# Optimization experiments

Hardware: AMD Instinct MI355X
Metric: run time of the kernel (lower is better)

Reference implementation:

```python
import jax, jax.numpy as jnp
import numpy as np

LN_EPS = 1e-5
DELTA_FACTOR = 0.01
PATCH_KH, PATCH_KW = 4, 4
SIGMA = 2.0


def layernorm(x, g, b):
    m = jnp.mean(x, axis=-1, keepdims=True)
    v = jnp.var(x, axis=-1, keepdims=True)
    return (x - m) * jax.lax.rsqrt(v + LN_EPS) * g + b


def grid_sample(src, grid):
    # src [B,C,H,W], grid [B,Hg,Wg,2] in [-1,1]; bilinear, align_corners=False, zero padding
    B, C, H, W = src.shape
    Hg, Wg = grid.shape[1], grid.shape[2]
    gx = (grid[..., 0] + 1.0) * (W * 0.5) - 0.5
    gy = (grid[..., 1] + 1.0) * (H * 0.5) - 0.5
    x0 = jnp.floor(gx)
    y0 = jnp.floor(gy)
    wx = gx - x0
    wy = gy - y0
    x0i = x0.astype(jnp.int32)
    y0i = y0.astype(jnp.int32)
    flat = src.reshape(B, C, H * W)

    def tap(xi, yi, w):
        valid = (xi >= 0) & (xi < W) & (yi >= 0) & (yi < H)
        idx = (jnp.clip(yi, 0, H - 1) * W + jnp.clip(xi, 0, W - 1)).reshape(B, -1)
        vals = jax.vmap(lambda f, i: f[:, i])(flat, idx)  # [B,C,Hg*Wg]
        return vals * (w * valid).reshape(B, 1, -1)

    out = (tap(x0i, y0i, (1 - wx) * (1 - wy)) + tap(x0i + 1, y0i, wx * (1 - wy))
           + tap(x0i, y0i + 1, (1 - wx) * wy) + tap(x0i + 1, y0i + 1, wx * wy))
    return out.reshape(B, C, Hg, Wg)


def gaussian_filt(x, k, sigma):
    # depthwise Gaussian blur, NCHW
    C = x.shape[1]
    coords = jnp.arange(k, dtype=x.dtype) - (k - 1) / 2.0
    g2 = jnp.exp(-(coords[:, None] ** 2 + coords[None, :] ** 2) / (2.0 * sigma ** 2))
    g2 = g2 / g2.sum()
    kern = jnp.broadcast_to(g2, (C, 1, k, k))
    p = (k - 1) // 2
    return jax.lax.conv_general_dilated(x, kern, (1, 1), [(p, p), (p, p)],
                                        dimension_numbers=('NCHW', 'OIHW', 'NCHW'),
                                        feature_group_count=C)


def reconstruct_feature(feature, mask, k, sigma):
    if k <= 1:
        return feature
    feature = feature * mask
    out = gaussian_filt(jnp.concatenate([feature, mask], axis=1), k, sigma)
    f_i = out[:, :-1]
    m_i = out[:, -1:]
    f_i = f_i / (m_i + 1e-6)
    f_i = f_i * (m_i > 0)
    return feature + (1 - mask) * f_i


def token2map(x, loc, H, W, k, sigma):
    B, N, C = x.shape
    l = jnp.clip(loc, 0.0, 1.0) * jnp.array([W - 1, H - 1], dtype=loc.dtype)
    l = jnp.round(l).astype(jnp.int32)
    idx = l[..., 0] + l[..., 1] * W + (jnp.arange(B, dtype=jnp.int32) * (H * W))[:, None]
    vals = jnp.concatenate([x, jnp.ones((B, N, 1), x.dtype)], axis=-1).reshape(B * N, C + 1)
    out = jnp.zeros((B * H * W, C + 1), x.dtype).at[idx.reshape(-1)].add(vals)
    out = out.reshape(B, H, W, C + 1).transpose(0, 3, 1, 2)
    feat, mask = out[:, :-1], out[:, -1:]
    feat = feat / (mask + 1e-6)
    mask = (mask > 0).astype(x.dtype)
    feat = feat * mask
    return reconstruct_feature(feat, mask, k, sigma)


def forward(x, loc, src, H, W, kernel_size,
            w_delta, b_delta, norm1_g, norm1_b, conv_w, conv_b,
            norm2_g, norm2_b, fc1_w, fc1_b, fc2_w, fc2_b):
    B, N, _ = loc.shape
    Cs, Hs, Ws = src.shape[1], src.shape[2], src.shape[3]
    delta = (layernorm(x, norm1_g, norm1_b) @ w_delta + b_delta) * DELTA_FACTOR
    loc_extra = jnp.clip(loc + delta, 0.0, 1.0)
    # extract_local_feature: 4x4 sub-pixel patch around each extra location
    xo = (jnp.arange(PATCH_KW, dtype=loc.dtype) - (PATCH_KW - 1) / 2.0) / (Ws - 1)
    yo = (jnp.arange(PATCH_KH, dtype=loc.dtype) - (PATCH_KH - 1) / 2.0) / (Hs - 1)
    off = jnp.stack([jnp.broadcast_to(xo[None, :], (PATCH_KH, PATCH_KW)),
                     jnp.broadcast_to(yo[:, None], (PATCH_KH, PATCH_KW))], axis=-1)
    grid = (loc_extra[:, :, None, None, :] + off[None, None]) * 2.0 - 1.0  # [B,N,kh,kw,2]
    patches = grid_sample(src, grid.reshape(B, N, PATCH_KH * PATCH_KW, 2))  # [B,C,N,kh*kw]
    patches = patches.reshape(B, Cs, N, PATCH_KH, PATCH_KW)
    # local_conv: 4x4 conv stride 4 over a 4x4 patch == single dot product
    extra = jnp.einsum('bcnhw,ochw->bno', patches, conv_w) + conv_b
    extra = layernorm(extra, norm2_g, norm2_b)
    # token2map scatter + gaussian reconstruction, then gather back at loc_extra
    fmap = token2map(x, loc, H, W, kernel_size, SIGMA)
    extra_inter = grid_sample(fmap, (loc_extra * 2.0 - 1.0)[:, None, :, :])  # [B,C,1,N]
    extra_inter = extra_inter[:, :, 0].transpose(0, 2, 1)  # [B,N,C]
    extra = jnp.concatenate([extra_inter, extra], axis=-1)
    h = jax.nn.gelu(extra @ fc1_w + fc1_b, approximate=False)
    extra = h @ fc2_w + fc2_b
    return jnp.concatenate([x, extra], axis=1), jnp.concatenate([loc, loc_extra], axis=1)


def setup_inputs() -> dict:
    key = jax.random.key(0)
    ks = jax.random.split(key, 12)
    B, N, D = 4, 16384, 256
    LD, HID = 64, 4 * D
    inp = {
        'x': jax.random.normal(ks[0], (B, N, D), jnp.float32),
        'loc': jax.random.uniform(ks[1], (B, N, 2), jnp.float32),
        'src': jax.random.normal(ks[2], (B, 3, 512, 512), jnp.float32),
        'pos_embed': jnp.zeros((1,), jnp.float32),
        'H': 128, 'W': 128, 'kernel_size': 3,
        'w_delta': jax.random.normal(ks[3], (D, 2), jnp.float32) * 0.02,
        'b_delta': jnp.zeros((2,), jnp.float32),
        'norm1_g': jnp.ones((D,), jnp.float32),
        'norm1_b': jnp.zeros((D,), jnp.float32),
        'conv_w': jax.random.normal(ks[4], (LD, 3, 4, 4), jnp.float32) * 0.1,
        'conv_b': jnp.zeros((LD,), jnp.float32),
        'norm2_g': jnp.ones((LD,), jnp.float32),
        'norm2_b': jnp.zeros((LD,), jnp.float32),
        'fc1_w': jax.random.normal(ks[5], (D + LD, HID), jnp.float32) * 0.02,
        'fc1_b': jnp.zeros((HID,), jnp.float32),
        'fc2_w': jax.random.normal(ks[6], (HID, D), jnp.float32) * 0.02,
        'fc2_b': jnp.zeros((D,), jnp.float32),
    }
    return inp


def reference(x, loc, src, pos_embed, H, W, kernel_size,
              w_delta, b_delta, norm1_g, norm1_b, conv_w, conv_b,
              norm2_g, norm2_b, fc1_w, fc1_b, fc2_w, fc2_b):
    # pos_embed is accepted by the torch forward but never used
    return forward(x, loc, src, H, W, kernel_size,
                   w_delta, b_delta, norm1_g, norm1_b, conv_w, conv_b,
                   norm2_g, norm2_b, fc1_w, fc1_b, fc2_w, fc2_b)
```

## Files before the change

kernel.cpp:

```cpp
#include <hip/hip_runtime.h>
#include <hip/hip_bf16.h>

#define B_    4
#define N_    16384
#define D_    256
#define LD_   64
#define HID_  1024
#define HW_   128
#define HSRC_ 512
#define CS_   3
#define KIN_  320

typedef __attribute__((ext_vector_type(8))) short bf16x8;
typedef __attribute__((ext_vector_type(4))) float f32x4;

__device__ __forceinline__ float wsum(float v) {
#pragma unroll
  for (int off = 32; off; off >>= 1) v += __shfl_xor(v, off, 64);
  return v;
}

__device__ __forceinline__ unsigned short f2bf(float f) {
  unsigned int u = __float_as_uint(f);
  u = (u + 0x7fffu + ((u >> 16) & 1u)) >> 16;
  return (unsigned short)u;
}

__global__ __launch_bounds__(256) void k_wconv(const float* __restrict__ fc1w,
                                               const float* __restrict__ fc2w,
                                               unsigned short* __restrict__ bt1,
                                               unsigned short* __restrict__ bt2) {
  int i = blockIdx.x * 256 + threadIdx.x;
  if (i < KIN_ * HID_) {
    int n = i / KIN_, k = i % KIN_;
    bt1[i] = f2bf(fc1w[(size_t)k * HID_ + n]);
  } else {
    int j = i - KIN_ * HID_;
    if (j < D_ * HID_) {
      int n = j / HID_, k = j % HID_;
      bt2[j] = f2bf(fc2w[(size_t)k * D_ + n]);
    }
  }
}

__global__ __launch_bounds__(256) void k_copy_x(const float* __restrict__ x,
                                                float* __restrict__ out0) {
  size_t i = (size_t)blockIdx.x * 256 + threadIdx.x;
  size_t e = i * 4;
  size_t b = e / ((size_t)N_ * D_);
  size_t off = e - b * (size_t)N_ * D_;
  *(float4*)(out0 + b * (size_t)2 * N_ * D_ + off) = *(const float4*)(x + e);
}

__global__ __launch_bounds__(256) void k_delta(const float* __restrict__ x,
                                               const float* __restrict__ loc,
                                               const float* __restrict__ wd,
                                               const float* __restrict__ bd,
                                               const float* __restrict__ g1,
                                               const float* __restrict__ b1,
                                               float* __restrict__ locex,
                                               float* __restrict__ out1) {
  int wv = threadIdx.x >> 6, lane = threadIdx.x & 63;
  int t = blockIdx.x * 4 + wv;
  const float4 xv = *(const float4*)(x + (size_t)t * D_ + lane * 4);
  float m = wsum(xv.x + xv.y + xv.z + xv.w) * (1.0f / D_);
  float d0 = xv.x - m, d1 = xv.y - m, d2 = xv.z - m, d3 = xv.w - m;
  float v = wsum(d0 * d0 + d1 * d1 + d2 * d2 + d3 * d3) * (1.0f / D_);
  float r = rsqrtf(v + 1e-5f);
  const float4 gv = *(const float4*)(g1 + lane * 4);
  const float4 bv = *(const float4*)(b1 + lane * 4);
  float n0 = d0 * r * gv.x + bv.x;
  float n1 = d1 * r * gv.y + bv.y;
  float n2 = d2 * r * gv.z + bv.z;
  float n3 = d3 * r * gv.w + bv.w;
  int i2 = lane * 8;
  float p0 = n0 * wd[i2 + 0] + n1 * wd[i2 + 2] + n2 * wd[i2 + 4] + n3 * wd[i2 + 6];
  float p1 = n0 * wd[i2 + 1] + n1 * wd[i2 + 3] + n2 * wd[i2 + 5] + n3 * wd[i2 + 7];
  p0 = wsum(p0);
  p1 = wsum(p1);
  if (lane == 0) {
    float lx = loc[(size_t)t * 2], ly = loc[(size_t)t * 2 + 1];
    float ex = fminf(fmaxf(lx + (p0 + bd[0]) * 0.01f, 0.0f), 1.0f);
    float ey = fminf(fmaxf(ly + (p1 + bd[1]) * 0.01f, 0.0f), 1.0f);
    locex[(size_t)t * 2] = ex;
    locex[(size_t)t * 2 + 1] = ey;
    int b = t >> 14, n = t & (N_ - 1);
    size_t o1 = (size_t)b * 2 * N_;
    out1[(o1 + n) * 2 + 0] = lx;
    out1[(o1 + n) * 2 + 1] = ly;
    out1[(o1 + N_ + n) * 2 + 0] = ex;
    out1[(o1 + N_ + n) * 2 + 1] = ey;
  }
}

__global__ __launch_bounds__(256) void k_build(const float* __restrict__ loc,
                                               int* __restrict__ head,
                                               int* __restrict__ nxt) {
  int t = blockIdx.x * 256 + threadIdx.x;
  int b = t >> 14;
  float lx = fminf(fmaxf(loc[(size_t)t * 2], 0.0f), 1.0f) * 127.0f;
  float ly = fminf(fmaxf(loc[(size_t)t * 2 + 1], 0.0f), 1.0f) * 127.0f;
  int ix = (int)rintf(lx);
  int iy = (int)rintf(ly);
  int cell = (b << 14) + iy * HW_ + ix;
  nxt[t] = atomicExch(head + cell, t);
}

__global__ __launch_bounds__(256) void k_gather(const float* __restrict__ x,
                                                const int* __restrict__ head,
                                                const int* __restrict__ nxt,
                                                float* __restrict__ featn,
                                                float* __restrict__ cntf) {
  int cell = blockIdx.x;
  int tid = threadIdx.x;
  __shared__ int toks[16];
  __shared__ int scount, snext;
  float acc = 0.0f;
  int total = 0;
  int cur = head[cell];
  while (cur >= 0) {
    if (tid == 0) {
      int c = 0, p = cur;
      while (p >= 0 && c < 16) {
        toks[c++] = p;
        p = nxt[p];
      }
      scount = c;
      snext = p;
    }
    __syncthreads();
    int c = scount;
    for (int i = 0; i < c; ++i) acc += x[(size_t)toks[i] * D_ + tid];
    total += c;
    cur = snext;
    __syncthreads();
  }
  featn[(size_t)cell * D_ + tid] = (total > 0) ? acc / ((float)total + 1e-6f) : 0.0f;
  if (tid == 0) cntf[cell] = (float)total;
}

__global__ __launch_bounds__(256) void k_filter(const float* __restrict__ featn,
                                                const float* __restrict__ cntf,
                                                float* __restrict__ fmap) {
  int pix = blockIdx.x;
  int c = threadIdx.x;
  int b = pix >> 14;
  int p = pix & 16383;
  int y = p >> 7, xc = p & 127;
  float cc = cntf[pix];
  float outv;
  if (cc > 0.0f) {
    outv = featn[(size_t)pix * D_ + c];
  } else {
    float e1 = expf(-0.125f), e2 = expf(-0.25f);
    float sumw = 1.0f + 4.0f * e1 + 4.0f * e2;
    float gf = 0.0f, gm = 0.0f;
#pragma unroll
    for (int dy = -1; dy <= 1; ++dy)
#pragma unroll
      for (int dx = -1; dx <= 1; ++dx) {
        int ny = y + dy, nx = xc + dx;
        if (ny < 0 || ny >= HW_ || nx < 0 || nx >= HW_) continue;
        int q = (b << 14) + ny * HW_ + nx;
        if (cntf[q] > 0.0f) {
          int dd = dy * dy + dx * dx;
          float w = (dd == 0 ? 1.0f : (dd == 1 ? e1 : e2)) / sumw;
          gf += w * featn[(size_t)q * D_ + c];
          gm += w;
        }
      }
    outv = (gm > 0.0f) ? gf / (gm + 1e-6f) : 0.0f;
  }
  fmap[(size_t)pix * D_ + c] = outv;
}

__global__ __launch_bounds__(256) void k_patch(const float* __restrict__ src,
                                               const float* __restrict__ locex,
                                               const float* __restrict__ convw,
                                               const float* __restrict__ convb,
                                               const float* __restrict__ g2,
                                               const float* __restrict__ b2,
                                               unsigned short* __restrict__ ecat) {
  __shared__ float cw[LD_ * 49];
  __shared__ float patch[4][48];
  for (int i = threadIdx.x; i < LD_ * 48; i += 256)
    cw[(i / 48) * 49 + (i % 48)] = convw[i];
  int wv = threadIdx.x >> 6, lane = threadIdx.x & 63;
  int t = blockIdx.x * 4 + wv;
  int b = t >> 14;
  float ex = locex[(size_t)t * 2], ey = locex[(size_t)t * 2 + 1];
  __syncthreads();
  if (lane < 48) {
    int c = lane >> 4, p = lane & 15, py = p >> 2, px = p & 3;
    float u = ex + ((float)px - 1.5f) / 511.0f;
    float vv = ey + ((float)py - 1.5f) / 511.0f;
    float gx = u * 512.0f - 0.5f;
    float gy = vv * 512.0f - 0.5f;
    float fx = floorf(gx), fy = floorf(gy);
    float wx = gx - fx, wy = gy - fy;
    int x0 = (int)fx, y0 = (int)fy;
    const float* plane = src + (size_t)(b * CS_ + c) * (HSRC_ * HSRC_);
    float acc = 0.0f;
#pragma unroll
    for (int ty = 0; ty < 2; ++ty)
#pragma unroll
      for (int tx = 0; tx < 2; ++tx) {
        int xi = x0 + tx, yi = y0 + ty;
        float w = (tx ? wx : 1.0f - wx) * (ty ? wy : 1.0f - wy);
        if (xi >= 0 && xi < HSRC_ && yi >= 0 && yi < HSRC_)
          acc += w * plane[yi * HSRC_ + xi];
      }
    patch[wv][lane] = acc;
  }
  __syncthreads();
  float e = convb[lane];
#pragma unroll
  for (int i = 0; i < 48; ++i) e += patch[wv][i] * cw[lane * 49 + i];
  float m = wsum(e) * (1.0f / 64.0f);
  float d = e - m;
  float v = wsum(d * d) * (1.0f / 64.0f);
  float val = d * rsqrtf(v + 1e-5f) * g2[lane] + b2[lane];
  ecat[(size_t)t * KIN_ + D_ + lane] = f2bf(val);
}

__global__ __launch_bounds__(256) void k_sample(const float* __restrict__ fmap,
                                                const float* __restrict__ locex,
                                                unsigned short* __restrict__ ecat) {
  int wv = threadIdx.x >> 6, lane = threadIdx.x & 63;
  int t = blockIdx.x * 4 + wv;
  int b = t >> 14;
  float gx = locex[(size_t)t * 2] * 128.0f - 0.5f;
  float gy = locex[(size_t)t * 2 + 1] * 128.0f - 0.5f;
  float fx = floorf(gx), fy = floorf(gy);
  float wx = gx - fx, wy = gy - fy;
  int x0 = (int)fx, y0 = (int)fy;
  const float* base = fmap + ((size_t)b << 14) * D_;
  float4 acc = {0.0f, 0.0f, 0.0f, 0.0f};
#pragma unroll
  for (int ty = 0; ty < 2; ++ty)
#pragma unroll
    for (int tx = 0; tx < 2; ++tx) {
      int xi = x0 + tx, yi = y0 + ty;
      float w = (tx ? wx : 1.0f - wx) * (ty ? wy : 1.0f - wy);
      if (xi >= 0 && xi < HW_ && yi >= 0 && yi < HW_) {
        const float4 f = *(const float4*)(base + (size_t)(yi * HW_ + xi) * D_ + lane * 4);
        acc.x += w * f.x;
        acc.y += w * f.y;
        acc.z += w * f.z;
        acc.w += w * f.w;
      }
    }
  ushort4 o;
  o.x = f2bf(acc.x);
  o.y = f2bf(acc.y);
  o.z = f2bf(acc.z);
  o.w = f2bf(acc.w);
  *(ushort4*)(ecat + (size_t)t * KIN_ + lane * 4) = o;
}

template <int GELU>
__global__ __launch_bounds__(256) void k_gemm(const unsigned short* __restrict__ A,
                                              const unsigned short* __restrict__ Bt,
                                              const float* __restrict__ bias, int K,
                                              int Nn, unsigned short* __restrict__ hout,
                                              float* __restrict__ out0) {
  __shared__ __align__(16) unsigned short As[64 * 40];
  __shared__ __align__(16) unsigned short Bs[64 * 40];
  int tid = threadIdx.x, wv = tid >> 6, lane = tid & 63;
  int tile_m = blockIdx.x * 64, tile_n = blockIdx.y * 64;
  int lr = tid >> 2, lc = (tid & 3) * 8;
  f32x4 acc[4];
#pragma unroll
  for (int s = 0; s < 4; ++s) acc[s] = (f32x4){0.0f, 0.0f, 0.0f, 0.0f};
  int arow = wv * 16 + (lane & 15);
  int kk = (lane >> 4) * 8;
  for (int k0 = 0; k0 < K; k0 += 32) {
    *(uint4*)(&As[lr * 40 + lc]) = *(const uint4*)(A + (size_t)(tile_m + lr) * K + k0 + lc);
    *(uint4*)(&Bs[lr * 40 + lc]) = *(const uint4*)(Bt + (size_t)(tile_n + lr) * K + k0 + lc);
    __syncthreads();
    bf16x8 af = *(const bf16x8*)(&As[arow * 40 + kk]);
#pragma unroll
    for (int s = 0; s < 4; ++s) {
      bf16x8 bfv = *(const bf16x8*)(&Bs[(s * 16 + (lane & 15)) * 40 + kk]);
      acc[s] = __builtin_amdgcn_mfma_f32_16x16x32_bf16(af, bfv, acc[s], 0, 0, 0);
    }
    __syncthreads();
  }
  int mbase = tile_m + wv * 16 + (lane >> 4) * 4;
#pragma unroll
  for (int s = 0; s < 4; ++s) {
    int n = tile_n + s * 16 + (lane & 15);
    float bv = bias[n];
#pragma unroll
    for (int r = 0; r < 4; ++r) {
      int m = mbase + r;
      float v = acc[s][r] + bv;
      if (GELU) {
        v = 0.5f * v * (1.0f + erff(v * 0.70710678118654752f));
        hout[(size_t)m * Nn + n] = f2bf(v);
      } else {
        int bb = m >> 14, ntok = m & (N_ - 1);
        out0[((size_t)bb * 2 * N_ + N_ + ntok) * D_ + n] = v;
      }
    }
  }
}

extern "C" void kernel_launch(void* const* d_in, const int* in_sizes, int n_in,
                              void* d_out, int out_size, void* d_ws, size_t ws_size,
                              hipStream_t stream) {
  const float* x = (const float*)d_in[0];
  const float* loc = (const float*)d_in[1];
  const float* src = (const float*)d_in[2];
  const float* wd = (const float*)d_in[7];
  const float* bd = (const float*)d_in[8];
  const float* g1 = (const float*)d_in[9];
  const float* b1 = (const float*)d_in[10];
  const float* cw = (const float*)d_in[11];
  const float* cb = (const float*)d_in[12];
  const float* g2 = (const float*)d_in[13];
  const float* b2 = (const float*)d_in[14];
  const float* fc1w = (const float*)d_in[15];
  const float* fc1b = (const float*)d_in[16];
  const float* fc2w = (const float*)d_in[17];
  const float* fc2b = (const float*)d_in[18];

  float* out0 = (float*)d_out;
  float* out1 = out0 + (size_t)B_ * 2 * N_ * D_;

  char* ws = (char*)d_ws;
  float* featn = (float*)(ws + 0);
  float* fmap = (float*)(ws + 67108864);
  unsigned short* h = (unsigned short*)(ws + 0);
  float* cntf = (float*)(ws + 134217728);
  float* locex = (float*)(ws + 134479872);
  unsigned short* ecat = (unsigned short*)(ws + 135004160);
  unsigned short* bt1 = (unsigned short*)(ws + 176947200);
  unsigned short* bt2 = (unsigned short*)(ws + 177602560);
  int* head = (int*)(ws + 178126848);
  int* nxt = (int*)(ws + 178388992);

  hipMemsetAsync(head, 0xFF, (size_t)262144, stream);

  k_wconv<<<2304, 256, 0, stream>>>(fc1w, fc2w, bt1, bt2);
  k_copy_x<<<16384, 256, 0, stream>>>(x, out0);
  k_delta<<<16384, 256, 0, stream>>>(x, loc, wd, bd, g1, b1, locex, out1);
  k_build<<<256, 256, 0, stream>>>(loc, head, nxt);
  k_gather<<<65536, 256, 0, stream>>>(x, head, nxt, featn, cntf);
  k_filter<<<65536, 256, 0, stream>>>(featn, cntf, fmap);
  k_patch<<<16384, 256, 0, stream>>>(src, locex, cw, cb, g2, b2, ecat);
  k_sample<<<16384, 256, 0, stream>>>(fmap, locex, ecat);
  k_gemm<1><<<dim3(1024, 16), 256, 0, stream>>>(ecat, bt1, fc1b, KIN_, HID_, h, nullptr);
  k_gemm<0><<<dim3(1024, 4), 256, 0, stream>>>(h, bt2, fc2b, HID_, D_, nullptr, out0);
}
```

Before: 665.4 us.

## Use 128x128 MFMA GEMM tiles with direct global-to-LDS loads and XCD-aware tile mapping

Replaces the 64x64 GEMM tile, where each wave computes a 16x64 strip, with a 128x128 tile in which each wave computes a 64x64 sub-block of 4x4 MFMA fragments. This raises arithmetic intensity per LDS load. Global-to-shared copies now use the global_load_lds builtin to skip register staging, and block indices are remapped so that consecutive M tiles land on the same XCD for L2 reuse. The trade-offs are higher register pressure and an unpadded LDS layout that may cause bank conflicts.

Result: faster. 592.0 us (-11.0%).

```diff
diff --git a/kernel.cpp b/kernel.cpp
--- a/kernel.cpp
+++ b/kernel.cpp
@@ -24,6 +24,12 @@
   unsigned int u = __float_as_uint(f);
   u = (u + 0x7fffu + ((u >> 16) & 1u)) >> 16;
   return (unsigned short)u;
+}
+
+__device__ __forceinline__ void async16(unsigned short* lds, const unsigned short* g) {
+  __builtin_amdgcn_global_load_lds(
+      (const __attribute__((address_space(1))) unsigned int*)g,
+      (__attribute__((address_space(3))) unsigned int*)lds, 16, 0, 0);
 }
 
 __global__ __launch_bounds__(256) void k_wconv(const float* __restrict__ fc1w,
@@ -259,48 +265,83 @@
 }
 
 template <int GELU>
-__global__ __launch_bounds__(256) void k_gemm(const unsigned short* __restrict__ A,
-                                              const unsigned short* __restrict__ Bt,
-                                              const float* __restrict__ bias, int K,
-                                              int Nn, unsigned short* __restrict__ hout,
-                                              float* __restrict__ out0) {
-  __shared__ __align__(16) unsigned short As[64 * 40];
-  __shared__ __align__(16) unsigned short Bs[64 * 40];
+__global__ __launch_bounds__(256) void k_gemm128(const unsigned short* __restrict__ A,
+                                                 const unsigned short* __restrict__ Bt,
+                                                 const float* __restrict__ bias, int K,
+                                                 int Nn, unsigned short* __restrict__ hout,
+                                                 float* __restrict__ out0) {
+  __shared__ __align__(16) unsigned short As[128 * 32];
+  __shared__ __align__(16) unsigned short Bs[128 * 32];
   int tid = threadIdx.x, wv = tid >> 6, lane = tid & 63;
-  int tile_m = blockIdx.x * 64, tile_n = blockIdx.y * 64;
-  int lr = tid >> 2, lc = (tid & 3) * 8;
-  f32x4 acc[4];
-#pragma unroll
-  for (int s = 0; s < 4; ++s) acc[s] = (f32x4){0.0f, 0.0f, 0.0f, 0.0f};
-  int arow = wv * 16 + (lane & 15);
+  int wm = wv & 1, wn = wv >> 1;
+
+  int nt_cnt = gridDim.x;
+  int lin = blockIdx.y * nt_cnt + blockIdx.x;
+  int xcd = lin & 7;
+  int slot = lin >> 3;
+  int tile_n = (slot % nt_cnt) * 128;
+  int tile_m = ((slot / nt_cnt) * 8 + xcd) * 128;
+
+  f32x4 acc[4][4];
+#pragma unroll
+  for (int i = 0; i < 4; ++i)
+#pragma unroll
+    for (int j = 0; j < 4; ++j) acc[i][j] = (f32x4){0.0f, 0.0f, 0.0f, 0.0f};
+
+  int r0 = tid >> 2, c0 = (tid & 3) * 8;
+  const unsigned short* ga = A + (size_t)(tile_m + r0) * K + c0;
+  const unsigned short* gb = Bt + (size_t)(tile_n + r0) * K + c0;
+  size_t rowskip = (size_t)64 * K;
+  unsigned short* lA0 = As + tid * 8;
+  unsigned short* lA1 = As + 2048 + tid * 8;
+  unsigned short* lB0 = Bs + tid * 8;
+  unsigned short* lB1 = Bs + 2048 + tid * 8;
+
+  int ar = wm * 64 + (lane & 15);
+  int br = wn * 64 + (lane & 15);
   int kk = (lane >> 4) * 8;
+
   for (int k0 = 0; k0 < K; k0 += 32) {
-    *(uint4*)(&As[lr * 40 + lc]) = *(const uint4*)(A + (size_t)(tile_m + lr) * K + k0 + lc);
-    *(uint4*)(&Bs[lr * 40 + lc]) = *(const uint4*)(Bt + (size_t)(tile_n + lr) * K + k0 + lc);
+    async16(lA0, ga);
+    async16(lA1, ga + rowskip);
+    async16(lB0, gb);
+    async16(lB1, gb + rowskip);
+    ga += 32;
+    gb += 32;
     __syncthreads();
-    bf16x8 af = *(const bf16x8*)(&As[arow * 40 + kk]);
-#pragma unroll
-    for (int s = 0; s < 4; ++s) {
-      bf16x8 bfv = *(const bf16x8*)(&Bs[(s * 16 + (lane & 15)) * 40 + kk]);
-      acc[s] = __builtin_amdgcn_mfma_f32_16x16x32_bf16(af, bfv, acc[s], 0, 0, 0);
-    }
+    bf16x8 afr[4], bfr[4];
+#pragma unroll
+    for (int i = 0; i < 4; ++i) {
+      afr[i] = *(const bf16x8*)(As + (ar + i * 16) * 32 + kk);
+      bfr[i] = *(const bf16x8*)(Bs + (br + i * 16) * 32 + kk);
+    }
+#pragma unroll
+    for (int mt = 0; mt < 4; ++mt)
+#pragma unroll
+      for (int nt = 0; nt < 4; ++nt)
+        acc[mt][nt] =
+            __builtin_amdgcn_mfma_f32_16x16x32_bf16(afr[mt], bfr[nt], acc[mt][nt], 0, 0, 0);
     __syncthreads();
   }
-  int mbase = tile_m + wv * 16 + (lane >> 4) * 4;
-#pragma unroll
-  for (int s = 0; s < 4; ++s) {
-    int n = tile_n + s * 16 + (lane & 15);
+
+#pragma unroll
+  for (int nt = 0; nt < 4; ++nt) {
+    int n = tile_n + wn * 64 + nt * 16 + (lane & 15);
     float bv = bias[n];
 #pragma unroll
-    for (int r = 0; r < 4; ++r) {
-      int m = mbase + r;
-      float v = acc[s][r] + bv;
-      if (GELU) {
-        v = 0.5f * v * (1.0f + erff(v * 0.70710678118654752f));
-        hout[(size_t)m * Nn + n] = f2bf(v);
-      } else {
-        int bb = m >> 14, ntok = m & (N_ - 1);
-        out0[((size_t)bb * 2 * N_ + N_ + ntok) * D_ + n] = v;
+    for (int mt = 0; mt < 4; ++mt) {
+      int mbase = tile_m + wm * 64 + mt * 16 + (lane >> 4) * 4;
+#pragma unroll
+      for (int r = 0; r < 4; ++r) {
+        int m = mbase + r;
+        float v = acc[mt][nt][r] + bv;
+        if (GELU) {
+          v = 0.5f * v * (1.0f + erff(v * 0.70710678118654752f));
+          hout[(size_t)m * Nn + n] = f2bf(v);
+        } else {
+          int bb = m >> 14, ntok = m & (N_ - 1);
+          out0[((size_t)bb * 2 * N_ + N_ + ntok) * D_ + n] = v;
+        }
       }
     }
   }
@@ -350,6 +391,6 @@
   k_filter<<<65536, 256, 0, stream>>>(featn, cntf, fmap);
   k_patch<<<16384, 256, 0, stream>>>(src, locex, cw, cb, g2, b2, ecat);
   k_sample<<<16384, 256, 0, stream>>>(fmap, locex, ecat);
-  k_gemm<1><<<dim3(1024, 16), 256, 0, stream>>>(ecat, bt1, fc1b, KIN_, HID_, h, nullptr);
-  k_gemm<0><<<dim3(1024, 4), 256, 0, stream>>>(h, bt2, fc2b, HID_, D_, nullptr, out0);
-}
+  k_gemm128<1><<<dim3(8, 512), 256, 0, stream>>>(ecat, bt1, fc1b, KIN_, HID_, h, nullptr);
+  k_gemm128<0><<<dim3(2, 512), 256, 0, stream>>>(h, bt2, fc2b, HID_, D_, nullptr, out0);
+}
```
